# Optimization experiments

Hardware: AMD Instinct MI355X
Metric: run time of the kernel (lower is better)

## Reference

```python
import jax, jax.numpy as jnp
import numpy as np

B_SZ, NP, NTOK, D, H, DH, D2 = 8192, 10, 21, 128, 2, 64, 32
EPS = 1e-8
PATCH_POS = np.array([2 * k - 1 for k in range(1, NP + 1)])  # [1,3,...,19]
STAT_POS = np.array([0] + [2 * k for k in range(1, NP + 1)])  # [0,2,...,20]


def setup_inputs() -> dict:
    key = jax.random.key(0)
    ks = jax.random.split(key, 12)
    x = jax.random.normal(ks[0], (B_SZ, NTOK, D), jnp.float32)
    # rotary frequencies: unit-magnitude complex exp(i * pos * theta)
    inv_freq = 1.0 / (10000.0 ** (jnp.arange(D2, dtype=jnp.float32) / D2))
    ang = jnp.arange(NTOK, dtype=jnp.float32)[:, None] * inv_freq[None, :]  # [N, d2]
    fc_real, fc_imag = jnp.cos(ang), jnp.sin(ang)
    s = 1.0 / np.sqrt(D)
    g = 1.0 + 0.02 * jax.random.normal(ks[1], (D,), jnp.float32)
    Wqkv = s * jax.random.normal(ks[2], (D, 3 * D), jnp.float32)
    bqkv = jnp.zeros((3 * D,), jnp.float32)
    Wout = s * jax.random.normal(ks[3], (D, D), jnp.float32)
    bout = jnp.zeros((D,), jnp.float32)
    Wg = s * jax.random.normal(ks[4], (D, D), jnp.float32)
    bg = jnp.zeros((D,), jnp.float32)
    Wr = s * jax.random.normal(ks[5], (D, D), jnp.float32)
    br = jnp.zeros((D,), jnp.float32)
    # learned bias B: decoupled init 0.0, coupled patch<->stat pairs 2.0
    Bb = np.zeros((NTOK, NTOK), np.float32)
    Bb[PATCH_POS, STAT_POS[1:]] = 2.0
    Bb[STAT_POS[1:], PATCH_POS] = 2.0
    return dict(x=x, fc_real=fc_real, fc_imag=fc_imag, g=g, Wqkv=Wqkv, bqkv=bqkv,
                Wout=Wout, bout=bout, Wg=Wg, bg=bg, Wr=Wr, br=br, Bbias=jnp.asarray(Bb))


def _zcrmsnorm(x, g):
    x0 = x - x.mean(-1, keepdims=True)
    return x0 / jnp.sqrt(jnp.mean(x0 * x0, -1, keepdims=True) + EPS) * g


def _rope(t, fr, fi):
    # t: [B,H,N,DH] viewed as complex pairs [B,H,N,d2,2]; fr/fi: [N,d2]
    tr = t.reshape(*t.shape[:-1], D2, 2)
    a, b = tr[..., 0], tr[..., 1]
    out = jnp.stack([a * fr - b * fi, a * fi + b * fr], axis=-1)
    return out.reshape(t.shape)


def reference(x, fc_real, fc_imag, g, Wqkv, bqkv, Wout, bout, Wg, bg, Wr, br, Bbias):
    B, N, Dm = x.shape
    h = _zcrmsnorm(x, g)
    qkv = (h @ Wqkv + bqkv).reshape(B, N, 3, H, DH)
    q = qkv[:, :, 0].transpose(0, 2, 1, 3)  # [B,H,N,DH]
    k = qkv[:, :, 1].transpose(0, 2, 1, 3)
    v = qkv[:, :, 2].transpose(0, 2, 1, 3)
    fr, fi = fc_real[:N], fc_imag[:N]
    q, k = _rope(q, fr, fi), _rope(k, fr, fi)
    scale = 1.0 / np.sqrt(DH)
    scores = jnp.einsum('bhnd,bhmd->bhnm', q, k) * scale + Bbias[None, None]
    a_full = jax.nn.softmax(scores, axis=-1)
    y_full = jnp.einsum('bhnm,bhmd->bhnd', a_full, v)
    y_full = y_full.transpose(0, 2, 1, 3).reshape(B, N, Dm) @ Wout + bout
    # patch -> stat attention
    q_p, k_s, v_s = q[:, :, PATCH_POS], k[:, :, STAT_POS], v[:, :, STAT_POS]
    sc2 = jnp.einsum('bhnd,bhmd->bhnm', q_p, k_s) * scale
    a2 = jax.nn.softmax(sc2, axis=-1)
    y2 = jnp.einsum('bhnm,bhmd->bhnd', a2, v_s).transpose(0, 2, 1, 3).reshape(B, NP, Dm)
    y2 = y2 @ Wr + br
    h_patch = h[:, PATCH_POS]  # [B,NP,D]
    norms = jnp.linalg.norm(h_patch, axis=-1, keepdims=True)
    uncertainty = 1.0 - jax.nn.sigmoid(norms - norms.mean())
    gate = jax.nn.sigmoid(h_patch @ Wg + bg) * uncertainty
    y = y_full.at[:, PATCH_POS, :].add(gate * y2)
    return x + y
```

## Files before the change

kernel.cpp:

```cpp
#include <hip/hip_runtime.h>
#include <math.h>

#define NB   8192
#define NTOK 21
#define NP   10

typedef __bf16 bf16_t;
typedef __bf16 bf16x8 __attribute__((ext_vector_type(8)));
typedef __bf16 bf16x4 __attribute__((ext_vector_type(4)));
typedef float  f32x4  __attribute__((ext_vector_type(4)));

#define ROW128(r,c) ((r)*128 + ((c) ^ (((r)&7)<<3)))
#define VTIDX(d,m)  ((d)*32  + ((m) ^ (((d)&3)<<3)))
#define ATIDX(r,m)  ((r)*32  + ((m) ^ (((r)&3)<<3)))

#define MFMA(a,b,c) __builtin_amdgcn_mfma_f32_16x16x32_bf16((a),(b),(c),0,0,0)

__global__ __launch_bounds__(256) void k_prep(
    const float* __restrict__ Wqkv, const float* __restrict__ Wout,
    const float* __restrict__ Wg,   const float* __restrict__ Wr,
    const float* __restrict__ x,    const float* __restrict__ g,
    bf16_t* __restrict__ wq, bf16_t* __restrict__ wo,
    bf16_t* __restrict__ wgb, bf16_t* __restrict__ wrb,
    float* __restrict__ part)
{
    __shared__ float sd[4];
    if (blockIdx.x < 384) {
        int i = blockIdx.x * 256 + threadIdx.x;
        if (i < 49152) {
            int k = i / 384, n = i - k * 384;
            wq[((k >> 3) * 384 + n) * 8 + (k & 7)] = (bf16_t)Wqkv[i];
        } else {
            int j = i - 49152;
            int sel = j >> 14;
            int t = j & 16383;
            int k = t >> 7, n = t & 127;
            const float* src = sel == 0 ? Wout : (sel == 1 ? Wg : Wr);
            bf16_t* dst = sel == 0 ? wo : (sel == 1 ? wgb : wrb);
            dst[((k >> 3) * 128 + n) * 8 + (k & 7)] = (bf16_t)src[t];
        }
    } else {
        const int nb = blockIdx.x - 384;
        const int wave = threadIdx.x >> 6, lane = threadIdx.x & 63;
        const float g0v = g[lane], g1v = g[lane + 64];
        float acc = 0.f;
        #pragma unroll
        for (int rr = 0; rr < 8; rr++) {
            int row = nb * 32 + wave * 8 + rr;
            int b = row / NP, p = row - b * NP;
            const float* xr = x + (size_t)b * 2688 + (2 * p + 1) * 128;
            float a0 = xr[lane], a1 = xr[lane + 64];
            float s = a0 + a1, sq = a0 * a0 + a1 * a1;
            #pragma unroll
            for (int off = 32; off; off >>= 1) { s += __shfl_xor(s, off); sq += __shfl_xor(sq, off); }
            float mean = s * (1.0f / 128);
            float rstd = rsqrtf(sq * (1.0f / 128) - mean * mean + 1e-8f);
            float h0 = (a0 - mean) * rstd * g0v;
            float h1 = (a1 - mean) * rstd * g1v;
            float n2 = h0 * h0 + h1 * h1;
            #pragma unroll
            for (int off = 32; off; off >>= 1) n2 += __shfl_xor(n2, off);
            if (lane == 0) acc += sqrtf(n2);
        }
        if (lane == 0) sd[wave] = acc;
        __syncthreads();
        if (threadIdx.x == 0)
            atomicAdd(&part[(nb & 63) * 16], sd[0] + sd[1] + sd[2] + sd[3]);
    }
}

__global__ __launch_bounds__(256, 4) void k_main(
    const float* __restrict__ x,   const float* __restrict__ fcr,
    const float* __restrict__ fci, const float* __restrict__ g,
    const float* __restrict__ bqkv, const float* __restrict__ bout,
    const float* __restrict__ bg,   const float* __restrict__ br,
    const float* __restrict__ Bb,   const float* __restrict__ part,
    const bf16_t* __restrict__ wq,  const bf16_t* __restrict__ wo,
    const bf16_t* __restrict__ wgb, const bf16_t* __restrict__ wrb,
    float* __restrict__ out)
{
    __shared__ __align__(16) bf16_t hsb[32 * 128];
    __shared__ __align__(16) bf16_t reg1[32 * 128];
    __shared__ __align__(16) bf16_t reg2[32 * 128];
    __shared__ __align__(16) bf16_t reg3[128 * 32];
    __shared__ __align__(16) char  pool[6144];
    __shared__ float normv[11];

    float* fcs  = (float*)pool;
    float* fis  = (float*)pool + 672;

    const int tid = threadIdx.x;
    const int w = tid >> 6, l = tid & 63, l15 = l & 15, gq = l >> 4;
    const int b = blockIdx.x;
    const float* xb = x + (size_t)b * 2688;

    {
        const float4* c4 = (const float4*)fcr; float4* dc = (float4*)fcs;
        const float4* i4 = (const float4*)fci; float4* di = (float4*)fis;
        if (tid < 168) { dc[tid] = c4[tid]; di[tid] = i4[tid]; }
        for (int i = tid; i < 11 * 128; i += 256)
            hsb[(21 + (i >> 7)) * 128 + (i & 127)] = (bf16_t)0.f;
        if (tid < 64) {
            float s = part[tid * 16];
            #pragma unroll
            for (int off = 32; off; off >>= 1) s += __shfl_xor(s, off);
            if (tid == 0) normv[10] = s * (1.f / 81920.f);
        }
        for (int r = w; r < 21; r += 4) {
            float a0 = xb[r * 128 + l], a1 = xb[r * 128 + 64 + l];
            float s = a0 + a1, sq = a0 * a0 + a1 * a1;
            #pragma unroll
            for (int off = 32; off; off >>= 1) { s += __shfl_xor(s, off); sq += __shfl_xor(sq, off); }
            float mean = s * (1.0f / 128);
            float rstd = rsqrtf(sq * (1.0f / 128) - mean * mean + 1e-8f);
            float h0 = (a0 - mean) * rstd * g[l];
            float h1 = (a1 - mean) * rstd * g[l + 64];
            hsb[ROW128(r, l)]      = (bf16_t)h0;
            hsb[ROW128(r, l + 64)] = (bf16_t)h1;
            if (r & 1) {
                float n2 = h0 * h0 + h1 * h1;
                #pragma unroll
                for (int off = 32; off; off >>= 1) n2 += __shfl_xor(n2, off);
                if (l == 0) normv[r >> 1] = sqrtf(n2);
            }
        }
    }
    __syncthreads();

    {
        bf16x8 afr[2][4];
        #pragma unroll
        for (int mt = 0; mt < 2; mt++)
            #pragma unroll
            for (int ks = 0; ks < 4; ks++)
                afr[mt][ks] = *(const bf16x8*)&hsb[ROW128(mt * 16 + l15, ks * 32 + gq * 8)];
        #pragma unroll 2
        for (int q6 = 0; q6 < 6; ++q6) {
            int nt = w * 6 + q6;
            int n = nt * 16 + l15;
            bf16x8 bfr[4];
            #pragma unroll
            for (int ks = 0; ks < 4; ks++)
                bfr[ks] = *(const bf16x8*)&wq[((ks * 4 + gq) * 384 + n) * 8];
            float bias = bqkv[n];
            #pragma unroll
            for (int mt = 0; mt < 2; mt++) {
                f32x4 acc = {0.f, 0.f, 0.f, 0.f};
                #pragma unroll
                for (int ks = 0; ks < 4; ks++) acc = MFMA(afr[mt][ks], bfr[ks], acc);
                int rbase = mt * 16 + gq * 4;
                if (n < 256) {
                    int d = n & 63, j = d >> 1;
                    bool ev = !(d & 1);
                    bf16_t* dst = (n < 128) ? reg1 : reg2;
                    int cc = n & 127;
                    #pragma unroll
                    for (int i = 0; i < 4; i++) {
                        int r = rbase + i; int rr = r < 21 ? r : 0;
                        float v = acc[i] + bias;
                        float p = __shfl_xor(v, 1);
                        float fr = fcs[rr * 32 + j], fi = fis[rr * 32 + j];
                        float o = ev ? (v * fr - p * fi) : (p * fi + v * fr);
                        dst[ROW128(r, cc)] = (bf16_t)o;
                    }
                } else {
                    int d = n - 256;
                    bf16x4 pv;
                    #pragma unroll
                    for (int i = 0; i < 4; i++) pv[i] = (bf16_t)(acc[i] + bias);
                    *(bf16x4*)&reg3[VTIDX(d, rbase)] = pv;
                }
            }
        }
    }
    __syncthreads();

    {
        bf16_t* attb  = (bf16_t*)pool;
        bf16_t* att2e = (bf16_t*)pool + 2048;
        {
            const int hh = w >> 1, mt = w & 1;
            f32x4 acc0 = {0.f, 0.f, 0.f, 0.f}, acc1 = {0.f, 0.f, 0.f, 0.f};
            #pragma unroll
            for (int ks = 0; ks < 2; ks++) {
                bf16x8 a  = *(const bf16x8*)&reg1[ROW128(mt * 16 + l15, hh * 64 + ks * 32 + gq * 8)];
                bf16x8 b0 = *(const bf16x8*)&reg2[ROW128(l15,           hh * 64 + ks * 32 + gq * 8)];
                bf16x8 b1 = *(const bf16x8*)&reg2[ROW128(16 + l15,      hh * 64 + ks * 32 + gq * 8)];
                acc0 = MFMA(a, b0, acc0);
                acc1 = MFMA(a, b1, acc1);
            }
            const int m0 = l15, m1 = 16 + l15;
            const bool c1 = (m1 < 21);
            #pragma unroll
            for (int i = 0; i < 4; i++) {
                int r = mt * 16 + gq * 4 + i;
                int rr = r < 21 ? r : 0;
                float v0 = acc0[i] * 0.125f + Bb[rr * 21 + m0];
                float v1 = c1 ? acc1[i] * 0.125f + Bb[rr * 21 + m1] : -1e30f;
                float mx = fmaxf(v0, v1);
                #pragma unroll
                for (int off = 8; off; off >>= 1) mx = fmaxf(mx, __shfl_xor(mx, off));
                float e0 = __expf(v0 - mx);
                float e1 = c1 ? __expf(v1 - mx) : 0.f;
                float s = e0 + e1;
                #pragma unroll
                for (int off = 8; off; off >>= 1) s += __shfl_xor(s, off);
                float is = 1.f / s;
                bool rv = (r < 21);
                attb[hh * 1024 + ATIDX(r, m0)] = (bf16_t)(rv ? e0 * is : 0.f);
                attb[hh * 1024 + ATIDX(r, m1)] = (bf16_t)(rv ? e1 * is : 0.f);
            }
        }
        if ((w & 1) == 0) {
            const int hh = w >> 1;
            int ra = 2 * l15 + 1; if (ra > 20) ra = 20;
            int rb = 2 * l15;     if (rb > 20) rb = 20;
            f32x4 acc = {0.f, 0.f, 0.f, 0.f};
            #pragma unroll
            for (int ks = 0; ks < 2; ks++) {
                bf16x8 a  = *(const bf16x8*)&reg1[ROW128(ra, hh * 64 + ks * 32 + gq * 8)];
                bf16x8 bb = *(const bf16x8*)&reg2[ROW128(rb, hh * 64 + ks * 32 + gq * 8)];
                acc = MFMA(a, bb, acc);
            }
            const bool cv = (l15 < 11);
            #pragma unroll
            for (int i = 0; i < 4; i++) {
                int p = gq * 4 + i;
                float v = cv ? acc[i] * 0.125f : -1e30f;
                float mx = v;
                #pragma unroll
                for (int off = 8; off; off >>= 1) mx = fmaxf(mx, __shfl_xor(mx, off));
                float e = cv ? __expf(v - mx) : 0.f;
                float s = e;
                #pragma unroll
                for (int off = 8; off; off >>= 1) s += __shfl_xor(s, off);
                float is = 1.f / s;
                att2e[hh * 512 + ATIDX(p, 2 * l15)]     = (bf16_t)((p < 10) ? e * is : 0.f);
                att2e[hh * 512 + ATIDX(p, 2 * l15 + 1)] = (bf16_t)0.f;
            }
        }
    }
    __syncthreads();

    {
        bf16_t* attb  = (bf16_t*)pool;
        bf16_t* att2e = (bf16_t*)pool + 2048;
        bf16_t* y2bb  = reg1;
        for (int t = w * 6; t < w * 6 + 6; ++t) {
            int hh, dloc, mt = 0, isY2;
            if (t < 16) { hh = t >> 3; mt = (t >> 2) & 1; dloc = hh * 64 + (t & 3) * 16 + l15; isY2 = 0; }
            else        { int u = t - 16; hh = u >> 2;    dloc = hh * 64 + (u & 3) * 16 + l15; isY2 = 1; }
            bf16x8 a;
            if (!isY2) { int r = mt * 16 + l15; a = *(const bf16x8*)&attb[hh * 1024 + ATIDX(r, gq * 8)]; }
            else       {                        a = *(const bf16x8*)&att2e[hh * 512 + ATIDX(l15, gq * 8)]; }
            bf16x8 bb = *(const bf16x8*)&reg3[VTIDX(dloc, gq * 8)];
            f32x4 acc = {0.f, 0.f, 0.f, 0.f};
            acc = MFMA(a, bb, acc);
            if (!isY2) {
                #pragma unroll
                for (int i = 0; i < 4; i++) reg2[ROW128(mt * 16 + gq * 4 + i, dloc)] = (bf16_t)acc[i];
            } else {
                #pragma unroll
                for (int i = 0; i < 4; i++) {
                    int rr2 = gq * 4 + i;
                    if (rr2 < 10) y2bb[ROW128(rr2, dloc)] = (bf16_t)acc[i];
                }
            }
        }
    }
    __syncthreads();

    {
        bf16_t* y2bb = reg1;
        float mn = normv[10];
        float* gyb = (float*)reg3;
        #pragma unroll
        for (int q2 = 0; q2 < 2; q2++) {
            int nt = w * 2 + q2;
            int n = nt * 16 + l15;
            int yrow = l15 < 10 ? l15 : 0;
            f32x4 accg = {0.f, 0.f, 0.f, 0.f}, accr = {0.f, 0.f, 0.f, 0.f};
            #pragma unroll
            for (int ks = 0; ks < 4; ks++) {
                bf16x8 wgf = *(const bf16x8*)&wgb[((ks * 4 + gq) * 128 + n) * 8];
                bf16x8 wrf = *(const bf16x8*)&wrb[((ks * 4 + gq) * 128 + n) * 8];
                bf16x8 ha  = *(const bf16x8*)&hsb[ROW128(2 * l15 + 1, ks * 32 + gq * 8)];
                bf16x8 ya  = *(const bf16x8*)&y2bb[ROW128(yrow, ks * 32 + gq * 8)];
                accg = MFMA(ha, wgf, accg);
                accr = MFMA(ya, wrf, accr);
            }
            float bgc = bg[n], brc = br[n];
            #pragma unroll
            for (int i = 0; i < 4; i++) {
                int p = gq * 4 + i;
                if (p < 10) {
                    float gate = 1.f / (1.f + __expf(-(accg[i] + bgc)));
                    float u = 1.f - 1.f / (1.f + __expf(-(normv[p] - mn)));
                    gyb[p * 128 + n] = u * gate * (accr[i] + brc);
                }
            }
        }
    }
    __syncthreads();

    {
        float* gyb = (float*)reg3;
        float* ob = out + (size_t)b * 2688;
        for (int t = w * 4; t < w * 4 + 4; ++t) {
            int mt = t >> 3, nt = t & 7;
            int n = nt * 16 + l15;
            f32x4 acc = {0.f, 0.f, 0.f, 0.f};
            #pragma unroll
            for (int ks = 0; ks < 4; ks++) {
                bf16x8 a  = *(const bf16x8*)&reg2[ROW128(mt * 16 + l15, ks * 32 + gq * 8)];
                bf16x8 wf = *(const bf16x8*)&wo[((ks * 4 + gq) * 128 + n) * 8];
                acc = MFMA(a, wf, acc);
            }
            float bo = bout[n];
            #pragma unroll
            for (int i = 0; i < 4; i++) {
                int r = mt * 16 + gq * 4 + i;
                if (r < 21) {
                    float v = xb[r * 128 + n] + acc[i] + bo;
                    if (r & 1) v += gyb[((r - 1) >> 1) * 128 + n];
                    ob[r * 128 + n] = v;
                }
            }
        }
    }
}

extern "C" void kernel_launch(void* const* d_in, const int* in_sizes, int n_in,
                              void* d_out, int out_size, void* d_ws, size_t ws_size,
                              hipStream_t stream)
{
    (void)in_sizes; (void)n_in; (void)out_size; (void)ws_size;
    const float* x    = (const float*)d_in[0];
    const float* fcr  = (const float*)d_in[1];
    const float* fci  = (const float*)d_in[2];
    const float* g    = (const float*)d_in[3];
    const float* Wqkv = (const float*)d_in[4];
    const float* bqkv = (const float*)d_in[5];
    const float* Wout = (const float*)d_in[6];
    const float* bout = (const float*)d_in[7];
    const float* Wg   = (const float*)d_in[8];
    const float* bg   = (const float*)d_in[9];
    const float* Wr   = (const float*)d_in[10];
    const float* br   = (const float*)d_in[11];
    const float* Bb   = (const float*)d_in[12];
    float* out = (float*)d_out;

    char* wsb = (char*)d_ws;
    float* part = (float*)wsb;
    bf16_t* wq  = (bf16_t*)(wsb + 4096);
    bf16_t* wo  = wq + 49152;
    bf16_t* wgb = wo + 16384;
    bf16_t* wrb = wgb + 16384;

    hipMemsetAsync(part, 0, 4096, stream);
    hipLaunchKernelGGL(k_prep, dim3(2944), dim3(256), 0, stream,
                       Wqkv, Wout, Wg, Wr, x, g, wq, wo, wgb, wrb, part);
    hipLaunchKernelGGL(k_main, dim3(NB),   dim3(256), 0, stream,
                       x, fcr, fci, g, bqkv, bout, bg, br, Bb, part, wq, wo, wgb, wrb, out);
}
```

Measured before the change: 369.1 us.

## Shrink LDS buffers to 24 token rows, switch to fp16 MFMA, raise occupancy

Token rows are now packed as two overlapping 16-row tiles starting at rows 0 and 8 instead of 0 and 16, so the shared buffers hold 24 rows instead of 32. Total LDS per block drops, and the launch bound goes from 4 to 5 blocks per CU. Operands switch from bf16 to fp16 MFMA, and the layernorm prologue now uses vectorized float4 loads with 16-lane groups. The overlapping tiles recompute rows 8-15 twice and store them twice, which is redundant work. fp16 may lose range compared with bf16.

```diff
diff --git a/kernel.cpp b/kernel.cpp
--- a/kernel.cpp
+++ b/kernel.cpp
@@ -5,23 +5,24 @@
 #define NTOK 21
 #define NP   10
 
-typedef __bf16 bf16_t;
-typedef __bf16 bf16x8 __attribute__((ext_vector_type(8)));
-typedef __bf16 bf16x4 __attribute__((ext_vector_type(4)));
-typedef float  f32x4  __attribute__((ext_vector_type(4)));
+typedef _Float16 f16_t;
+typedef _Float16 f16x8 __attribute__((ext_vector_type(8)));
+typedef _Float16 f16x4 __attribute__((ext_vector_type(4)));
+typedef float    f32x4 __attribute__((ext_vector_type(4)));
 
 #define ROW128(r,c) ((r)*128 + ((c) ^ (((r)&7)<<3)))
 #define VTIDX(d,m)  ((d)*32  + ((m) ^ (((d)&3)<<3)))
 #define ATIDX(r,m)  ((r)*32  + ((m) ^ (((r)&3)<<3)))
-
-#define MFMA(a,b,c) __builtin_amdgcn_mfma_f32_16x16x32_bf16((a),(b),(c),0,0,0)
+#define TOK0(mt)    ((mt) ? 8 : 0)
+
+#define MFMA(a,b,c) __builtin_amdgcn_mfma_f32_16x16x32_f16((a),(b),(c),0,0,0)
 
 __global__ __launch_bounds__(256) void k_prep(
     const float* __restrict__ Wqkv, const float* __restrict__ Wout,
     const float* __restrict__ Wg,   const float* __restrict__ Wr,
     const float* __restrict__ x,    const float* __restrict__ g,
-    bf16_t* __restrict__ wq, bf16_t* __restrict__ wo,
-    bf16_t* __restrict__ wgb, bf16_t* __restrict__ wrb,
+    f16_t* __restrict__ wq, f16_t* __restrict__ wo,
+    f16_t* __restrict__ wgb, f16_t* __restrict__ wrb,
     float* __restrict__ part)
 {
     __shared__ float sd[4];
@@ -29,15 +30,15 @@
         int i = blockIdx.x * 256 + threadIdx.x;
         if (i < 49152) {
             int k = i / 384, n = i - k * 384;
-            wq[((k >> 3) * 384 + n) * 8 + (k & 7)] = (bf16_t)Wqkv[i];
+            wq[((k >> 3) * 384 + n) * 8 + (k & 7)] = (f16_t)Wqkv[i];
         } else {
             int j = i - 49152;
             int sel = j >> 14;
             int t = j & 16383;
             int k = t >> 7, n = t & 127;
             const float* src = sel == 0 ? Wout : (sel == 1 ? Wg : Wr);
-            bf16_t* dst = sel == 0 ? wo : (sel == 1 ? wgb : wrb);
-            dst[((k >> 3) * 128 + n) * 8 + (k & 7)] = (bf16_t)src[t];
+            f16_t* dst = sel == 0 ? wo : (sel == 1 ? wgb : wrb);
+            dst[((k >> 3) * 128 + n) * 8 + (k & 7)] = (f16_t)src[t];
         }
     } else {
         const int nb = blockIdx.x - 384;
@@ -69,21 +70,21 @@
     }
 }
 
-__global__ __launch_bounds__(256, 4) void k_main(
+__global__ __launch_bounds__(256, 5) void k_main(
     const float* __restrict__ x,   const float* __restrict__ fcr,
     const float* __restrict__ fci, const float* __restrict__ g,
     const float* __restrict__ bqkv, const float* __restrict__ bout,
     const float* __restrict__ bg,   const float* __restrict__ br,
     const float* __restrict__ Bb,   const float* __restrict__ part,
-    const bf16_t* __restrict__ wq,  const bf16_t* __restrict__ wo,
-    const bf16_t* __restrict__ wgb, const bf16_t* __restrict__ wrb,
+    const f16_t* __restrict__ wq,  const f16_t* __restrict__ wo,
+    const f16_t* __restrict__ wgb, const f16_t* __restrict__ wrb,
     float* __restrict__ out)
 {
-    __shared__ __align__(16) bf16_t hsb[32 * 128];
-    __shared__ __align__(16) bf16_t reg1[32 * 128];
-    __shared__ __align__(16) bf16_t reg2[32 * 128];
-    __shared__ __align__(16) bf16_t reg3[128 * 32];
-    __shared__ __align__(16) char  pool[6144];
+    __shared__ __align__(16) f16_t hsb[24 * 128];
+    __shared__ __align__(16) f16_t reg1[24 * 128];
+    __shared__ __align__(16) f16_t reg2[24 * 128];
+    __shared__ __align__(16) f16_t reg3[128 * 32];
+    __shared__ __align__(16) char  pool[5376];
     __shared__ float normv[11];
 
     float* fcs  = (float*)pool;
@@ -98,61 +99,84 @@
         const float4* c4 = (const float4*)fcr; float4* dc = (float4*)fcs;
         const float4* i4 = (const float4*)fci; float4* di = (float4*)fis;
         if (tid < 168) { dc[tid] = c4[tid]; di[tid] = i4[tid]; }
-        for (int i = tid; i < 11 * 128; i += 256)
-            hsb[(21 + (i >> 7)) * 128 + (i & 127)] = (bf16_t)0.f;
+        f16x8 zz;
+        #pragma unroll
+        for (int j = 0; j < 8; j++) zz[j] = (f16_t)0.f;
+        {
+            f16x8* z = (f16x8*)reg3;
+            z[tid] = zz; z[tid + 256] = zz;
+        }
+        if (tid < 48) {
+            int r = 21 + (tid >> 4), c0 = (tid & 15) * 8;
+            *(f16x8*)&hsb[ROW128(r, c0)] = zz;
+        }
         if (tid < 64) {
             float s = part[tid * 16];
             #pragma unroll
             for (int off = 32; off; off >>= 1) s += __shfl_xor(s, off);
             if (tid == 0) normv[10] = s * (1.f / 81920.f);
         }
-        for (int r = w; r < 21; r += 4) {
-            float a0 = xb[r * 128 + l], a1 = xb[r * 128 + 64 + l];
-            float s = a0 + a1, sq = a0 * a0 + a1 * a1;
-            #pragma unroll
-            for (int off = 32; off; off >>= 1) { s += __shfl_xor(s, off); sq += __shfl_xor(sq, off); }
+        const int gid = tid >> 4, lane16 = tid & 15;
+        const int c0 = lane16 * 8;
+        float4 ga = *(const float4*)&g[c0];
+        float4 gb4 = *(const float4*)&g[c0 + 4];
+        for (int r = gid; r < 21; r += 16) {
+            float4 a4 = *(const float4*)&xb[r * 128 + c0];
+            float4 b4 = *(const float4*)&xb[r * 128 + c0 + 4];
+            float s  = a4.x + a4.y + a4.z + a4.w + b4.x + b4.y + b4.z + b4.w;
+            float sq = a4.x*a4.x + a4.y*a4.y + a4.z*a4.z + a4.w*a4.w
+                     + b4.x*b4.x + b4.y*b4.y + b4.z*b4.z + b4.w*b4.w;
+            #pragma unroll
+            for (int off = 8; off; off >>= 1) { s += __shfl_xor(s, off); sq += __shfl_xor(sq, off); }
             float mean = s * (1.0f / 128);
             float rstd = rsqrtf(sq * (1.0f / 128) - mean * mean + 1e-8f);
-            float h0 = (a0 - mean) * rstd * g[l];
-            float h1 = (a1 - mean) * rstd * g[l + 64];
-            hsb[ROW128(r, l)]      = (bf16_t)h0;
-            hsb[ROW128(r, l + 64)] = (bf16_t)h1;
+            float h[8];
+            h[0]=(a4.x-mean)*rstd*ga.x;  h[1]=(a4.y-mean)*rstd*ga.y;
+            h[2]=(a4.z-mean)*rstd*ga.z;  h[3]=(a4.w-mean)*rstd*ga.w;
+            h[4]=(b4.x-mean)*rstd*gb4.x; h[5]=(b4.y-mean)*rstd*gb4.y;
+            h[6]=(b4.z-mean)*rstd*gb4.z; h[7]=(b4.w-mean)*rstd*gb4.w;
+            f16x8 hv;
+            #pragma unroll
+            for (int j = 0; j < 8; j++) hv[j] = (f16_t)h[j];
+            *(f16x8*)&hsb[ROW128(r, c0)] = hv;
             if (r & 1) {
-                float n2 = h0 * h0 + h1 * h1;
-                #pragma unroll
-                for (int off = 32; off; off >>= 1) n2 += __shfl_xor(n2, off);
-                if (l == 0) normv[r >> 1] = sqrtf(n2);
-            }
-        }
-    }
-    __syncthreads();
-
-    {
-        bf16x8 afr[2][4];
+                float n2 = 0.f;
+                #pragma unroll
+                for (int j = 0; j < 8; j++) n2 += h[j] * h[j];
+                #pragma unroll
+                for (int off = 8; off; off >>= 1) n2 += __shfl_xor(n2, off);
+                if (lane16 == 0) normv[r >> 1] = sqrtf(n2);
+            }
+        }
+    }
+    __syncthreads();
+
+    {
+        f16x8 afr[2][4];
         #pragma unroll
         for (int mt = 0; mt < 2; mt++)
             #pragma unroll
             for (int ks = 0; ks < 4; ks++)
-                afr[mt][ks] = *(const bf16x8*)&hsb[ROW128(mt * 16 + l15, ks * 32 + gq * 8)];
+                afr[mt][ks] = *(const f16x8*)&hsb[ROW128(TOK0(mt) + l15, ks * 32 + gq * 8)];
         #pragma unroll 2
         for (int q6 = 0; q6 < 6; ++q6) {
             int nt = w * 6 + q6;
             int n = nt * 16 + l15;
-            bf16x8 bfr[4];
+            f16x8 bfr[4];
             #pragma unroll
             for (int ks = 0; ks < 4; ks++)
-                bfr[ks] = *(const bf16x8*)&wq[((ks * 4 + gq) * 384 + n) * 8];
+                bfr[ks] = *(const f16x8*)&wq[((ks * 4 + gq) * 384 + n) * 8];
             float bias = bqkv[n];
             #pragma unroll
             for (int mt = 0; mt < 2; mt++) {
                 f32x4 acc = {0.f, 0.f, 0.f, 0.f};
                 #pragma unroll
                 for (int ks = 0; ks < 4; ks++) acc = MFMA(afr[mt][ks], bfr[ks], acc);
-                int rbase = mt * 16 + gq * 4;
+                int rbase = TOK0(mt) + gq * 4;
                 if (n < 256) {
                     int d = n & 63, j = d >> 1;
                     bool ev = !(d & 1);
-                    bf16_t* dst = (n < 128) ? reg1 : reg2;
+                    f16_t* dst = (n < 128) ? reg1 : reg2;
                     int cc = n & 127;
                     #pragma unroll
                     for (int i = 0; i < 4; i++) {
@@ -161,14 +185,14 @@
                         float p = __shfl_xor(v, 1);
                         float fr = fcs[rr * 32 + j], fi = fis[rr * 32 + j];
                         float o = ev ? (v * fr - p * fi) : (p * fi + v * fr);
-                        dst[ROW128(r, cc)] = (bf16_t)o;
+                        dst[ROW128(r, cc)] = (f16_t)o;
                     }
                 } else {
                     int d = n - 256;
-                    bf16x4 pv;
+                    f16x4 pv;
                     #pragma unroll
-                    for (int i = 0; i < 4; i++) pv[i] = (bf16_t)(acc[i] + bias);
-                    *(bf16x4*)&reg3[VTIDX(d, rbase)] = pv;
+                    for (int i = 0; i < 4; i++) pv[i] = (f16_t)(acc[i] + bias);
+                    *(f16x4*)&reg3[VTIDX(d, rbase)] = pv;
                 }
             }
         }
@@ -176,16 +200,17 @@
     __syncthreads();
 
     {
-        bf16_t* attb  = (bf16_t*)pool;
-        bf16_t* att2e = (bf16_t*)pool + 2048;
+        f16_t* attb  = (f16_t*)pool;
+        f16_t* att2e = (f16_t*)pool + 1536;
         {
             const int hh = w >> 1, mt = w & 1;
+            const int b1row = (16 + l15 < 21) ? 16 + l15 : 20;
             f32x4 acc0 = {0.f, 0.f, 0.f, 0.f}, acc1 = {0.f, 0.f, 0.f, 0.f};
             #pragma unroll
             for (int ks = 0; ks < 2; ks++) {
-                bf16x8 a  = *(const bf16x8*)&reg1[ROW128(mt * 16 + l15, hh * 64 + ks * 32 + gq * 8)];
-                bf16x8 b0 = *(const bf16x8*)&reg2[ROW128(l15,           hh * 64 + ks * 32 + gq * 8)];
-                bf16x8 b1 = *(const bf16x8*)&reg2[ROW128(16 + l15,      hh * 64 + ks * 32 + gq * 8)];
+                f16x8 a  = *(const f16x8*)&reg1[ROW128(TOK0(mt) + l15, hh * 64 + ks * 32 + gq * 8)];
+                f16x8 b0 = *(const f16x8*)&reg2[ROW128(l15,            hh * 64 + ks * 32 + gq * 8)];
+                f16x8 b1 = *(const f16x8*)&reg2[ROW128(b1row,          hh * 64 + ks * 32 + gq * 8)];
                 acc0 = MFMA(a, b0, acc0);
                 acc1 = MFMA(a, b1, acc1);
             }
@@ -193,7 +218,7 @@
             const bool c1 = (m1 < 21);
             #pragma unroll
             for (int i = 0; i < 4; i++) {
-                int r = mt * 16 + gq * 4 + i;
+                int r = TOK0(mt) + gq * 4 + i;
                 int rr = r < 21 ? r : 0;
                 float v0 = acc0[i] * 0.125f + Bb[rr * 21 + m0];
                 float v1 = c1 ? acc1[i] * 0.125f + Bb[rr * 21 + m1] : -1e30f;
@@ -207,8 +232,8 @@
                 for (int off = 8; off; off >>= 1) s += __shfl_xor(s, off);
                 float is = 1.f / s;
                 bool rv = (r < 21);
-                attb[hh * 1024 + ATIDX(r, m0)] = (bf16_t)(rv ? e0 * is : 0.f);
-                attb[hh * 1024 + ATIDX(r, m1)] = (bf16_t)(rv ? e1 * is : 0.f);
+                attb[hh * 768 + ATIDX(r, m0)] = (f16_t)(rv ? e0 * is : 0.f);
+                attb[hh * 768 + ATIDX(r, m1)] = (f16_t)(rv ? e1 * is : 0.f);
             }
         }
         if ((w & 1) == 0) {
@@ -218,8 +243,8 @@
             f32x4 acc = {0.f, 0.f, 0.f, 0.f};
             #pragma unroll
             for (int ks = 0; ks < 2; ks++) {
-                bf16x8 a  = *(const bf16x8*)&reg1[ROW128(ra, hh * 64 + ks * 32 + gq * 8)];
-                bf16x8 bb = *(const bf16x8*)&reg2[ROW128(rb, hh * 64 + ks * 32 + gq * 8)];
+                f16x8 a  = *(const f16x8*)&reg1[ROW128(ra, hh * 64 + ks * 32 + gq * 8)];
+                f16x8 bb = *(const f16x8*)&reg2[ROW128(rb, hh * 64 + ks * 32 + gq * 8)];
                 acc = MFMA(a, bb, acc);
             }
             const bool cv = (l15 < 11);
@@ -235,35 +260,35 @@
                 #pragma unroll
                 for (int off = 8; off; off >>= 1) s += __shfl_xor(s, off);
                 float is = 1.f / s;
-                att2e[hh * 512 + ATIDX(p, 2 * l15)]     = (bf16_t)((p < 10) ? e * is : 0.f);
-                att2e[hh * 512 + ATIDX(p, 2 * l15 + 1)] = (bf16_t)0.f;
-            }
-        }
-    }
-    __syncthreads();
-
-    {
-        bf16_t* attb  = (bf16_t*)pool;
-        bf16_t* att2e = (bf16_t*)pool + 2048;
-        bf16_t* y2bb  = reg1;
+                att2e[hh * 512 + ATIDX(p, 2 * l15)]     = (f16_t)((p < 10) ? e * is : 0.f);
+                att2e[hh * 512 + ATIDX(p, 2 * l15 + 1)] = (f16_t)0.f;
+            }
+        }
+    }
+    __syncthreads();
+
+    {
+        f16_t* attb  = (f16_t*)pool;
+        f16_t* att2e = (f16_t*)pool + 1536;
+        f16_t* y2bb  = reg1;
         for (int t = w * 6; t < w * 6 + 6; ++t) {
             int hh, dloc, mt = 0, isY2;
             if (t < 16) { hh = t >> 3; mt = (t >> 2) & 1; dloc = hh * 64 + (t & 3) * 16 + l15; isY2 = 0; }
             else        { int u = t - 16; hh = u >> 2;    dloc = hh * 64 + (u & 3) * 16 + l15; isY2 = 1; }
-            bf16x8 a;
-            if (!isY2) { int r = mt * 16 + l15; a = *(const bf16x8*)&attb[hh * 1024 + ATIDX(r, gq * 8)]; }
-            else       {                        a = *(const bf16x8*)&att2e[hh * 512 + ATIDX(l15, gq * 8)]; }
-            bf16x8 bb = *(const bf16x8*)&reg3[VTIDX(dloc, gq * 8)];
+            f16x8 a;
+            if (!isY2) { int r = TOK0(mt) + l15; a = *(const f16x8*)&attb[hh * 768 + ATIDX(r, gq * 8)]; }
+            else       {                         a = *(const f16x8*)&att2e[hh * 512 + ATIDX(l15, gq * 8)]; }
+            f16x8 bb = *(const f16x8*)&reg3[VTIDX(dloc, gq * 8)];
             f32x4 acc = {0.f, 0.f, 0.f, 0.f};
             acc = MFMA(a, bb, acc);
             if (!isY2) {
                 #pragma unroll
-                for (int i = 0; i < 4; i++) reg2[ROW128(mt * 16 + gq * 4 + i, dloc)] = (bf16_t)acc[i];
+                for (int i = 0; i < 4; i++) reg2[ROW128(TOK0(mt) + gq * 4 + i, dloc)] = (f16_t)acc[i];
             } else {
                 #pragma unroll
                 for (int i = 0; i < 4; i++) {
                     int rr2 = gq * 4 + i;
-                    if (rr2 < 10) y2bb[ROW128(rr2, dloc)] = (bf16_t)acc[i];
+                    if (rr2 < 10) y2bb[ROW128(rr2, dloc)] = (f16_t)acc[i];
                 }
             }
         }
@@ -271,7 +296,7 @@
     __syncthreads();
 
     {
-        bf16_t* y2bb = reg1;
+        f16_t* y2bb = reg1;
         float mn = normv[10];
         float* gyb = (float*)reg3;
         #pragma unroll
@@ -279,13 +304,14 @@
             int nt = w * 2 + q2;
             int n = nt * 16 + l15;
             int yrow = l15 < 10 ? l15 : 0;
+            int hr   = l15 < 10 ? 2 * l15 + 1 : 1;
             f32x4 accg = {0.f, 0.f, 0.f, 0.f}, accr = {0.f, 0.f, 0.f, 0.f};
             #pragma unroll
             for (int ks = 0; ks < 4; ks++) {
-                bf16x8 wgf = *(const bf16x8*)&wgb[((ks * 4 + gq) * 128 + n) * 8];
-                bf16x8 wrf = *(const bf16x8*)&wrb[((ks * 4 + gq) * 128 + n) * 8];
-                bf16x8 ha  = *(const bf16x8*)&hsb[ROW128(2 * l15 + 1, ks * 32 + gq * 8)];
-                bf16x8 ya  = *(const bf16x8*)&y2bb[ROW128(yrow, ks * 32 + gq * 8)];
+                f16x8 wgf = *(const f16x8*)&wgb[((ks * 4 + gq) * 128 + n) * 8];
+                f16x8 wrf = *(const f16x8*)&wrb[((ks * 4 + gq) * 128 + n) * 8];
+                f16x8 ha  = *(const f16x8*)&hsb[ROW128(hr, ks * 32 + gq * 8)];
+                f16x8 ya  = *(const f16x8*)&y2bb[ROW128(yrow, ks * 32 + gq * 8)];
                 accg = MFMA(ha, wgf, accg);
                 accr = MFMA(ya, wrf, accr);
             }
@@ -312,14 +338,14 @@
             f32x4 acc = {0.f, 0.f, 0.f, 0.f};
             #pragma unroll
             for (int ks = 0; ks < 4; ks++) {
-                bf16x8 a  = *(const bf16x8*)&reg2[ROW128(mt * 16 + l15, ks * 32 + gq * 8)];
-                bf16x8 wf = *(const bf16x8*)&wo[((ks * 4 + gq) * 128 + n) * 8];
+                f16x8 a  = *(const f16x8*)&reg2[ROW128(TOK0(mt) + l15, ks * 32 + gq * 8)];
+                f16x8 wf = *(const f16x8*)&wo[((ks * 4 + gq) * 128 + n) * 8];
                 acc = MFMA(a, wf, acc);
             }
             float bo = bout[n];
             #pragma unroll
             for (int i = 0; i < 4; i++) {
-                int r = mt * 16 + gq * 4 + i;
+                int r = TOK0(mt) + gq * 4 + i;
                 if (r < 21) {
                     float v = xb[r * 128 + n] + acc[i] + bo;
                     if (r & 1) v += gyb[((r - 1) >> 1) * 128 + n];
@@ -352,10 +378,10 @@
 
     char* wsb = (char*)d_ws;
     float* part = (float*)wsb;
-    bf16_t* wq  = (bf16_t*)(wsb + 4096);
-    bf16_t* wo  = wq + 49152;
-    bf16_t* wgb = wo + 16384;
-    bf16_t* wrb = wgb + 16384;
+    f16_t* wq  = (f16_t*)(wsb + 4096);
+    f16_t* wo  = wq + 49152;
+    f16_t* wgb = wo + 16384;
+    f16_t* wrb = wgb + 16384;
 
     hipMemsetAsync(part, 0, 4096, stream);
     hipLaunchKernelGGL(k_prep, dim3(2944), dim3(256), 0, stream,
```

New measurement: 389.9 us. +5.7%, slower.
